# Kernel optimization log

Hardware: AMD Instinct MI355X
Metric: run time of the kernel (lower is better)

## Reference

```python
import jax, jax.numpy as jnp
import numpy as np

N_HEADS = 16
D_EMBED = 1024
D_HEAD = D_EMBED // N_HEADS
CAUSAL = True


def setup_inputs() -> dict:
    key = jax.random.key(0)
    k1, k2, k3, k4, k5 = jax.random.split(key, 5)
    B, S = 2, 2048
    scale = 1.0 / np.sqrt(D_EMBED)
    return {
        "x": jax.random.normal(k1, (B, S, D_EMBED), dtype=jnp.float32),
        "Wqkv": jax.random.normal(k2, (D_EMBED, 3 * D_EMBED), dtype=jnp.float32) * scale,
        "bqkv": jax.random.normal(k3, (3 * D_EMBED,), dtype=jnp.float32) * 0.01,
        "Wo": jax.random.normal(k4, (D_EMBED, D_EMBED), dtype=jnp.float32) * scale,
        "bo": jax.random.normal(k5, (D_EMBED,), dtype=jnp.float32) * 0.01,
    }


def reference(x, Wqkv, bqkv, Wo, bo):
    B, S, D = x.shape
    qkv = x @ Wqkv + bqkv                      # [B,S,3D]
    q, k, v = jnp.split(qkv, 3, axis=-1)
    # [B,S,D] -> [B,H,S,dh]
    def heads(t):
        return t.reshape(B, S, N_HEADS, D_HEAD).transpose(0, 2, 1, 3)
    q, k, v = heads(q), heads(k), heads(v)
    scores = jnp.einsum('bhqd,bhkd->bhqk', q, k)
    if CAUSAL:
        mask = jnp.triu(jnp.ones((S, S), dtype=bool), k=1)  # True above diagonal
        scores = jnp.where(mask, -jnp.inf, scores)
    scores = scores / jnp.sqrt(jnp.asarray(D_HEAD, dtype=scores.dtype))
    attn = jax.nn.softmax(scores, axis=-1)
    out = jnp.einsum('bhqk,bhkd->bhqd', attn, v)           # [B,H,S,dh]
    out = out.transpose(0, 2, 1, 3).reshape(B, S, D)
    return out @ Wo + bo
```

## Files before the change

kernel.cpp:

```cpp
#include <hip/hip_runtime.h>
#include <hip/hip_bf16.h>
#include <cstdint>
#include <cstddef>


using bf16 = __hip_bfloat16;
typedef __attribute__((ext_vector_type(8))) short short8;
typedef __attribute__((ext_vector_type(4))) float f32x4;
typedef __attribute__((ext_vector_type(16))) float f32x16;
typedef __attribute__((ext_vector_type(4))) unsigned int u32x4;

__device__ __forceinline__ unsigned short f2b(float f) {
    bf16 h = __float2bfloat16(f);
    return *reinterpret_cast<unsigned short*>(&h);
}

__device__ __forceinline__ void async16(const void* g, void* l) {
    __builtin_amdgcn_global_load_lds(
        (const __attribute__((address_space(1))) void*)g,
        (__attribute__((address_space(3))) void*)l, 16, 0, 0);
}

__global__ __launch_bounds__(256) void prep_kernel(
    const float* __restrict__ x, bf16* __restrict__ x_bf,
    const float* __restrict__ Wqkv, bf16* __restrict__ wqkv_t,
    const float* __restrict__ Wo, bf16* __restrict__ wo_t) {
    const int bid = blockIdx.x;
    const int tid = threadIdx.x;
    if (bid < 4096) {
        const int i = bid * 256 + tid;
        const float4 v = reinterpret_cast<const float4*>(x)[i];
        ushort4 o;
        o.x = f2b(v.x); o.y = f2b(v.y); o.z = f2b(v.z); o.w = f2b(v.w);
        reinterpret_cast<ushort4*>(x_bf)[i] = o;
        return;
    }
    __shared__ float tile[32][33];
    const float* in;
    bf16* out;
    int K, N, n0, k0;
    if (bid < 4096 + 3072) {
        const int blk = bid - 4096;
        in = Wqkv; out = wqkv_t; K = 1024; N = 3072;
        n0 = (blk % 96) * 32; k0 = (blk / 96) * 32;
    } else {
        const int blk = bid - 7168;
        in = Wo; out = wo_t; K = 1024; N = 1024;
        n0 = (blk % 32) * 32; k0 = (blk / 32) * 32;
    }
    const int tx = tid & 31, ty = tid >> 5;
    #pragma unroll
    for (int i = 0; i < 32; i += 8)
        tile[ty + i][tx] = in[(size_t)(k0 + ty + i) * N + n0 + tx];
    __syncthreads();
    #pragma unroll
    for (int i = 0; i < 32; i += 8)
        out[(size_t)(n0 + ty + i) * K + k0 + tx] = __float2bfloat16(tile[tx][ty + i]);
}

template <int EPI, int BN>
__global__ __launch_bounds__(256) void gemm_bt(
    const bf16* __restrict__ A,
    const bf16* __restrict__ Bt,
    const float* __restrict__ bias,
    float* __restrict__ Cf,
    bf16* __restrict__ qd, bf16* __restrict__ kd, bf16* __restrict__ vtd,
    int M, int N, int K) {
    constexpr int NFR = BN / 32;
    __shared__ bf16 As[2][128 * 32];
    __shared__ bf16 Bs[2][BN * 32];
    const int t = threadIdx.x;
    const int lane = t & 63;
    const int lr = lane & 15, lg = lane >> 4;
    const int wave = t >> 6;
    const int wr = wave >> 1, wc = wave & 1;
    const int m0 = blockIdx.x * 128, n0 = blockIdx.y * BN;

    const bf16* aSrc = A + (size_t)(m0 + (t >> 2)) * K + (t & 3) * 8;
    const bf16* bSrc = Bt + (size_t)(n0 + (t >> 2)) * K + (t & 3) * 8;
    const size_t rowStep = (size_t)64 * K;

    auto stage = [&](int buf, int k0) {
        async16(aSrc + k0, &As[buf][t * 8]);
        async16(aSrc + rowStep + k0, &As[buf][2048 + t * 8]);
        async16(bSrc + k0, &Bs[buf][t * 8]);
        if constexpr (BN == 128)
            async16(bSrc + rowStep + k0, &Bs[buf][2048 + t * 8]);
    };

    f32x4 acc[4][NFR] = {};

    stage(0, 0);
    __syncthreads();

    int cur = 0;
    for (int k0 = 0; k0 < K; k0 += 32) {
        if (k0 + 32 < K) stage(cur ^ 1, k0 + 32);
        short8 af[4], bfr[NFR];
        #pragma unroll
        for (int i = 0; i < 4; ++i)
            af[i] = *reinterpret_cast<const short8*>(
                &As[cur][(wr * 64 + i * 16 + lr) * 32 + lg * 8]);
        #pragma unroll
        for (int i = 0; i < NFR; ++i)
            bfr[i] = *reinterpret_cast<const short8*>(
                &Bs[cur][(wc * (BN / 2) + i * 16 + lr) * 32 + lg * 8]);
        #pragma unroll
        for (int mi = 0; mi < 4; ++mi)
            #pragma unroll
            for (int ni = 0; ni < NFR; ++ni)
                acc[mi][ni] = __builtin_amdgcn_mfma_f32_16x16x32_bf16(
                    af[mi], bfr[ni], acc[mi][ni], 0, 0, 0);
        __syncthreads();
        cur ^= 1;
    }

    #pragma unroll
    for (int mi = 0; mi < 4; ++mi) {
        #pragma unroll
        for (int ni = 0; ni < NFR; ++ni) {
            const int rowb = m0 + wr * 64 + mi * 16 + lg * 4;
            const int col = n0 + wc * (BN / 2) + ni * 16 + lr;
            if constexpr (EPI == 0) {
                #pragma unroll
                for (int r = 0; r < 4; ++r)
                    Cf[(size_t)(rowb + r) * N + col] = acc[mi][ni][r] + bias[col];
            } else {
                const float bs = bias[col];
                const int part = col >> 10;
                const int within = col & 1023;
                const int h = within >> 6, d = within & 63;
                const int b = rowb >> 11, s0 = rowb & 2047;
                const int bh = b * 16 + h;
                if (part == 2) {
                    ushort4 pk;
                    pk.x = f2b(acc[mi][ni][0] + bs);
                    pk.y = f2b(acc[mi][ni][1] + bs);
                    pk.z = f2b(acc[mi][ni][2] + bs);
                    pk.w = f2b(acc[mi][ni][3] + bs);
                    *reinterpret_cast<ushort4*>(
                        &vtd[((size_t)bh * 64 + d) * 2048 + s0]) = pk;
                } else {
                    bf16* dst = (part == 0) ? qd : kd;
                    #pragma unroll
                    for (int r = 0; r < 4; ++r)
                        dst[((size_t)bh * 2048 + s0 + r) * 64 + d] =
                            __float2bfloat16(acc[mi][ni][r] + bs);
                }
            }
        }
    }
}

__global__ __launch_bounds__(256, 2) void attn_kernel(const bf16* __restrict__ q,
                                                      const bf16* __restrict__ k,
                                                      const bf16* __restrict__ vt,
                                                      bf16* __restrict__ o) {
    const int S = 2048;
    const int f = blockIdx.x;
    const int res = f & 7, m = f >> 3;
    const int grp = m >> 4;
    const int bh = res + 8 * grp;
    const int bxr = m & 15;
    const int bx = (grp & 2) ? (15 - bxr) : bxr;
    const int b = bh >> 4, h = bh & 15;
    const int w = threadIdx.x >> 6;
    const int u = w >> 1, par = w & 1;
    const int lane = threadIdx.x & 63;
    const int ln = lane & 31;
    const int hi = lane >> 5;
    const int P = 2 * (15 - bx) + u;
    const int qbaseA = P * 64;
    const int qbaseB = P * 64 + 32;

    const bf16* qp = q + (size_t)bh * S * 64;
    const bf16* kp = k + (size_t)bh * S * 64;
    const bf16* vp = vt + (size_t)bh * 64 * S;

    short8 qfA[4], qfB[4];
    #pragma unroll
    for (int i = 0; i < 4; ++i) {
        qfA[i] = *reinterpret_cast<const short8*>(
            &qp[(size_t)(qbaseA + ln) * 64 + i * 16 + hi * 8]);
        qfB[i] = *reinterpret_cast<const short8*>(
            &qp[(size_t)(qbaseB + ln) * 64 + i * 16 + hi * 8]);
    }

    f32x16 oA0 = {}, oA1 = {}, oB0 = {}, oB1 = {};
    f32x4 lsvA = {0.f, 0.f, 0.f, 0.f}, lsvB = {0.f, 0.f, 0.f, 0.f};

    short8 kA[4], kB[4], vA[4], vB[4];

    auto kload = [&](short8 (&kf)[4], int tile) {
        const bf16* base = &kp[(size_t)(tile * 32 + ln) * 64 + hi * 8];
        #pragma unroll
        for (int i = 0; i < 4; ++i)
            kf[i] = *reinterpret_cast<const short8*>(base + i * 16);
    };
    auto vload = [&](short8 (&vf)[4], int tile) {
        #pragma unroll
        for (int dblk = 0; dblk < 2; ++dblk)
            #pragma unroll
            for (int half = 0; half < 2; ++half)
                vf[dblk * 2 + half] = *reinterpret_cast<const short8*>(
                    &vp[(size_t)(dblk * 32 + ln) * S + tile * 32 + half * 16 +
                        hi * 8]);
    };

    auto body = [&](const short8 (&kf)[4], const short8 (&vf)[4],
                    const short8 (&qf)[4], f32x16& o0, f32x16& o1, f32x4& lsv,
                    bool diag) {
        f32x16 z0 = {}, z1 = {};
        z0 = __builtin_amdgcn_mfma_f32_32x32x16_bf16(kf[0], qf[0], z0, 0, 0, 0);
        z0 = __builtin_amdgcn_mfma_f32_32x32x16_bf16(kf[1], qf[1], z0, 0, 0, 0);
        z1 = __builtin_amdgcn_mfma_f32_32x32x16_bf16(kf[2], qf[2], z1, 0, 0, 0);
        z1 = __builtin_amdgcn_mfma_f32_32x32x16_bf16(kf[3], qf[3], z1, 0, 0, 0);
        const f32x16 z = z0 + z1;
        f32x16 pv;
        #pragma unroll
        for (int rr = 0; rr < 16; ++rr) {
            const int kreg = (rr & 3) + 8 * (rr >> 2) + 4 * hi;
            float e = __expf(z[rr] * 0.125f);
            if (diag && (kreg > ln)) e = 0.f;
            pv[rr] = e;
            lsv[rr & 3] += e;
        }
        unsigned a0, a1, b0, b1, c0, c1, d0, d1;
        asm("v_cvt_pk_bf16_f32 %0, %1, %2" : "=v"(a0) : "v"(pv[0]), "v"(pv[1]));
        asm("v_cvt_pk_bf16_f32 %0, %1, %2" : "=v"(a1) : "v"(pv[2]), "v"(pv[3]));
        asm("v_cvt_pk_bf16_f32 %0, %1, %2" : "=v"(b0) : "v"(pv[4]), "v"(pv[5]));
        asm("v_cvt_pk_bf16_f32 %0, %1, %2" : "=v"(b1) : "v"(pv[6]), "v"(pv[7]));
        asm("v_cvt_pk_bf16_f32 %0, %1, %2" : "=v"(c0) : "v"(pv[8]), "v"(pv[9]));
        asm("v_cvt_pk_bf16_f32 %0, %1, %2" : "=v"(c1) : "v"(pv[10]), "v"(pv[11]));
        asm("v_cvt_pk_bf16_f32 %0, %1, %2" : "=v"(d0) : "v"(pv[12]), "v"(pv[13]));
        asm("v_cvt_pk_bf16_f32 %0, %1, %2" : "=v"(d1) : "v"(pv[14]), "v"(pv[15]));
        asm("v_permlane32_swap_b32 %0, %1" : "+v"(a0), "+v"(b0));
        asm("v_permlane32_swap_b32 %0, %1" : "+v"(a1), "+v"(b1));
        asm("v_permlane32_swap_b32 %0, %1" : "+v"(c0), "+v"(d0));
        asm("v_permlane32_swap_b32 %0, %1" : "+v"(c1), "+v"(d1));
        u32x4 t0, t1;
        t0[0] = a0; t0[1] = a1; t0[2] = b0; t0[3] = b1;
        t1[0] = c0; t1[1] = c1; t1[2] = d0; t1[3] = d1;
        const short8 pa0 = __builtin_bit_cast(short8, t0);
        const short8 pa1 = __builtin_bit_cast(short8, t1);
        o0 = __builtin_amdgcn_mfma_f32_32x32x16_bf16(pa0, vf[0], o0, 0, 0, 0);
        o0 = __builtin_amdgcn_mfma_f32_32x32x16_bf16(pa1, vf[1], o0, 0, 0, 0);
        o1 = __builtin_amdgcn_mfma_f32_32x32x16_bf16(pa0, vf[2], o1, 0, 0, 0);
        o1 = __builtin_amdgcn_mfma_f32_32x32x16_bf16(pa1, vf[3], o1, 0, 0, 0);
    };

    auto dual = [&](const short8 (&kf)[4], const short8 (&vf)[4]) {
        body(kf, vf, qfA, oA0, oA1, lsvA, false);
        body(kf, vf, qfB, oB0, oB1, lsvB, false);
    };
    auto final_body = [&](const short8 (&kf)[4], const short8 (&vf)[4]) {
        if (par == 0) {
            body(kf, vf, qfA, oA0, oA1, lsvA, true);
            body(kf, vf, qfB, oB0, oB1, lsvB, false);
        } else {
            body(kf, vf, qfB, oB0, oB1, lsvB, true);
        }
    };

    kload(kA, par);
    vload(vA, par);
    int i = 0;
    for (; i + 2 <= P; i += 2) {
        kload(kB, par + 2 * (i + 1));
        vload(vB, par + 2 * (i + 1));
        dual(kA, vA);
        kload(kA, par + 2 * (i + 2));
        vload(vA, par + 2 * (i + 2));
        dual(kB, vB);
    }
    if (i < P) {
        kload(kB, par + 2 * P);
        vload(vB, par + 2 * P);
        dual(kA, vA);
        final_body(kB, vB);
    } else {
        final_body(kA, vA);
    }

    float lsA = (lsvA[0] + lsvA[1]) + (lsvA[2] + lsvA[3]);
    float lsB = (lsvB[0] + lsvB[1]) + (lsvB[2] + lsvB[3]);

    __shared__ float red[2][64][65];
    __shared__ float redl[2][64][2];
    if (par == 1) {
        float* dst = red[u][lane];
        #pragma unroll
        for (int rr = 0; rr < 16; ++rr) {
            dst[rr] = oA0[rr];
            dst[16 + rr] = oA1[rr];
            dst[32 + rr] = oB0[rr];
            dst[48 + rr] = oB1[rr];
        }
        redl[u][lane][0] = lsA;
        redl[u][lane][1] = lsB;
    }
    __syncthreads();
    if (par == 1) return;
    {
        const float* src = red[u][lane];
        #pragma unroll
        for (int rr = 0; rr < 16; ++rr) {
            oA0[rr] += src[rr];
            oA1[rr] += src[16 + rr];
            oB0[rr] += src[32 + rr];
            oB1[rr] += src[48 + rr];
        }
        lsA += redl[u][lane][0];
        lsB += redl[u][lane][1];
    }

    lsA += __shfl_xor(lsA, 32, 64);
    lsB += __shfl_xor(lsB, 32, 64);
    const float myInvA = 1.0f / lsA;
    const float myInvB = 1.0f / lsB;
    #pragma unroll
    for (int rr = 0; rr < 16; ++rr) {
        const int qrow = (rr & 3) + 8 * (rr >> 2) + 4 * hi;
        const float invA = __shfl(myInvA, qrow, 64);
        const float invB = __shfl(myInvB, qrow, 64);
        const size_t rowA = ((size_t)b * S + qbaseA + qrow) * 1024 + h * 64;
        const size_t rowB = ((size_t)b * S + qbaseB + qrow) * 1024 + h * 64;
        o[rowA + ln] = __float2bfloat16(oA0[rr] * invA);
        o[rowA + 32 + ln] = __float2bfloat16(oA1[rr] * invA);
        o[rowB + ln] = __float2bfloat16(oB0[rr] * invB);
        o[rowB + 32 + ln] = __float2bfloat16(oB1[rr] * invB);
    }
}

extern "C" void kernel_launch(void* const* d_in, const int* in_sizes, int n_in,
                              void* d_out, int out_size, void* d_ws, size_t ws_size,
                              hipStream_t stream) {
    const float* x = (const float*)d_in[0];
    const float* Wqkv = (const float*)d_in[1];
    const float* bqkv = (const float*)d_in[2];
    const float* Wo = (const float*)d_in[3];
    const float* bo = (const float*)d_in[4];
    float* out = (float*)d_out;
    char* ws = (char*)d_ws;

    bf16* x_bf = (bf16*)(ws);
    bf16* wqkv_t = (bf16*)(ws + 8388608);
    bf16* wo_t = (bf16*)(ws + 14680064);
    bf16* qb = (bf16*)(ws + 16777216);
    bf16* kb = (bf16*)(ws + 25165824);
    bf16* vtb = (bf16*)(ws + 33554432);
    bf16* attn_o = x_bf;

    prep_kernel<<<8192, 256, 0, stream>>>(x, x_bf, Wqkv, wqkv_t, Wo, wo_t);
    gemm_bt<1, 128><<<dim3(32, 24), 256, 0, stream>>>(
        x_bf, wqkv_t, bqkv, nullptr, qb, kb, vtb, 4096, 3072, 1024);
    attn_kernel<<<512, 256, 0, stream>>>(qb, kb, vtb, attn_o);
    gemm_bt<0, 64><<<dim3(32, 16), 256, 0, stream>>>(
        attn_o, wo_t, bo, out, nullptr, nullptr, nullptr, 4096, 1024, 1024);
}
```

Before: 106.8 us.

## Fold softmax scale into Q weights and compute row sums via MFMA

Pre-scales the Q columns of Wqkv and the Q bias by log2(e)/sqrt(64), so the attention kernel can call exp2f directly with no multiply. The row sums of the softmax are now computed by extra MFMAs against a vector of bf16 ones instead of VALU adds. This also removes the shuffle-based normalization and folds the sums into the shared-memory reduction. It adds two MFMAs per tile and rounds P to bf16 inside the sum, which changes numerics slightly.

```diff
diff --git a/kernel.cpp b/kernel.cpp
--- a/kernel.cpp
+++ b/kernel.cpp
@@ -9,6 +9,8 @@
 typedef __attribute__((ext_vector_type(4))) float f32x4;
 typedef __attribute__((ext_vector_type(16))) float f32x16;
 typedef __attribute__((ext_vector_type(4))) unsigned int u32x4;
+
+#define QSCALE 0.18033688f
 
 __device__ __forceinline__ unsigned short f2b(float f) {
     bf16 h = __float2bfloat16(f);
@@ -48,6 +50,8 @@
         in = Wo; out = wo_t; K = 1024; N = 1024;
         n0 = (blk % 32) * 32; k0 = (blk / 32) * 32;
     }
+    const float scl =
+        (bid >= 4096 && bid < 7168 && ((bid - 4096) % 96) < 32) ? QSCALE : 1.0f;
     const int tx = tid & 31, ty = tid >> 5;
     #pragma unroll
     for (int i = 0; i < 32; i += 8)
@@ -55,7 +59,8 @@
     __syncthreads();
     #pragma unroll
     for (int i = 0; i < 32; i += 8)
-        out[(size_t)(n0 + ty + i) * K + k0 + tx] = __float2bfloat16(tile[tx][ty + i]);
+        out[(size_t)(n0 + ty + i) * K + k0 + tx] =
+            __float2bfloat16(tile[tx][ty + i] * scl);
 }
 
 template <int EPI, int BN>
@@ -126,7 +131,8 @@
                 for (int r = 0; r < 4; ++r)
                     Cf[(size_t)(rowb + r) * N + col] = acc[mi][ni][r] + bias[col];
             } else {
-                const float bs = bias[col];
+                float bs = bias[col];
+                if (col < 1024) bs *= QSCALE;
                 const int part = col >> 10;
                 const int within = col & 1023;
                 const int h = within >> 6, d = within & 63;
@@ -186,8 +192,12 @@
             &qp[(size_t)(qbaseB + ln) * 64 + i * 16 + hi * 8]);
     }
 
+    short8 ones8;
+    #pragma unroll
+    for (int i = 0; i < 8; ++i) ones8[i] = (short)0x3F80;
+
     f32x16 oA0 = {}, oA1 = {}, oB0 = {}, oB1 = {};
-    f32x4 lsvA = {0.f, 0.f, 0.f, 0.f}, lsvB = {0.f, 0.f, 0.f, 0.f};
+    f32x16 lsA = {}, lsB = {};
 
     short8 kA[4], kB[4], vA[4], vB[4];
 
@@ -208,7 +218,7 @@
     };
 
     auto body = [&](const short8 (&kf)[4], const short8 (&vf)[4],
-                    const short8 (&qf)[4], f32x16& o0, f32x16& o1, f32x4& lsv,
+                    const short8 (&qf)[4], f32x16& o0, f32x16& o1, f32x16& ls,
                     bool diag) {
         f32x16 z0 = {}, z1 = {};
         z0 = __builtin_amdgcn_mfma_f32_32x32x16_bf16(kf[0], qf[0], z0, 0, 0, 0);
@@ -220,10 +230,9 @@
         #pragma unroll
         for (int rr = 0; rr < 16; ++rr) {
             const int kreg = (rr & 3) + 8 * (rr >> 2) + 4 * hi;
-            float e = __expf(z[rr] * 0.125f);
+            float e = exp2f(z[rr]);
             if (diag && (kreg > ln)) e = 0.f;
             pv[rr] = e;
-            lsv[rr & 3] += e;
         }
         unsigned a0, a1, b0, b1, c0, c1, d0, d1;
         asm("v_cvt_pk_bf16_f32 %0, %1, %2" : "=v"(a0) : "v"(pv[0]), "v"(pv[1]));
@@ -247,18 +256,20 @@
         o0 = __builtin_amdgcn_mfma_f32_32x32x16_bf16(pa1, vf[1], o0, 0, 0, 0);
         o1 = __builtin_amdgcn_mfma_f32_32x32x16_bf16(pa0, vf[2], o1, 0, 0, 0);
         o1 = __builtin_amdgcn_mfma_f32_32x32x16_bf16(pa1, vf[3], o1, 0, 0, 0);
+        ls = __builtin_amdgcn_mfma_f32_32x32x16_bf16(pa0, ones8, ls, 0, 0, 0);
+        ls = __builtin_amdgcn_mfma_f32_32x32x16_bf16(pa1, ones8, ls, 0, 0, 0);
     };
 
     auto dual = [&](const short8 (&kf)[4], const short8 (&vf)[4]) {
-        body(kf, vf, qfA, oA0, oA1, lsvA, false);
-        body(kf, vf, qfB, oB0, oB1, lsvB, false);
+        body(kf, vf, qfA, oA0, oA1, lsA, false);
+        body(kf, vf, qfB, oB0, oB1, lsB, false);
     };
     auto final_body = [&](const short8 (&kf)[4], const short8 (&vf)[4]) {
         if (par == 0) {
-            body(kf, vf, qfA, oA0, oA1, lsvA, true);
-            body(kf, vf, qfB, oB0, oB1, lsvB, false);
+            body(kf, vf, qfA, oA0, oA1, lsA, true);
+            body(kf, vf, qfB, oB0, oB1, lsB, false);
         } else {
-            body(kf, vf, qfB, oB0, oB1, lsvB, true);
+            body(kf, vf, qfB, oB0, oB1, lsB, true);
         }
     };
 
@@ -282,11 +293,7 @@
         final_body(kA, vA);
     }
 
-    float lsA = (lsvA[0] + lsvA[1]) + (lsvA[2] + lsvA[3]);
-    float lsB = (lsvB[0] + lsvB[1]) + (lsvB[2] + lsvB[3]);
-
-    __shared__ float red[2][64][65];
-    __shared__ float redl[2][64][2];
+    __shared__ float red[2][64][97];
     if (par == 1) {
         float* dst = red[u][lane];
         #pragma unroll
@@ -295,9 +302,9 @@
             dst[16 + rr] = oA1[rr];
             dst[32 + rr] = oB0[rr];
             dst[48 + rr] = oB1[rr];
-        }
-        redl[u][lane][0] = lsA;
-        redl[u][lane][1] = lsB;
+            dst[64 + rr] = lsA[rr];
+            dst[80 + rr] = lsB[rr];
+        }
     }
     __syncthreads();
     if (par == 1) return;
@@ -309,20 +316,16 @@
             oA1[rr] += src[16 + rr];
             oB0[rr] += src[32 + rr];
             oB1[rr] += src[48 + rr];
-        }
-        lsA += redl[u][lane][0];
-        lsB += redl[u][lane][1];
-    }
-
-    lsA += __shfl_xor(lsA, 32, 64);
-    lsB += __shfl_xor(lsB, 32, 64);
-    const float myInvA = 1.0f / lsA;
-    const float myInvB = 1.0f / lsB;
+            lsA[rr] += src[64 + rr];
+            lsB[rr] += src[80 + rr];
+        }
+    }
+
     #pragma unroll
     for (int rr = 0; rr < 16; ++rr) {
         const int qrow = (rr & 3) + 8 * (rr >> 2) + 4 * hi;
-        const float invA = __shfl(myInvA, qrow, 64);
-        const float invB = __shfl(myInvB, qrow, 64);
+        const float invA = 1.0f / lsA[rr];
+        const float invB = 1.0f / lsB[rr];
         const size_t rowA = ((size_t)b * S + qbaseA + qrow) * 1024 + h * 64;
         const size_t rowB = ((size_t)b * S + qbaseB + qrow) * 1024 + h * 64;
         o[rowA + ln] = __float2bfloat16(oA0[rr] * invA);
```

Result: slower. 114.5 us (+7.1%).
